# Kernel tuning notes

Measured on AMD Instinct MI355X. Metric: run time of the kernel, lower is better.

## Reference

```python
import jax, jax.numpy as jnp
import numpy as np

B, S, D = 4, 2048, 512
H = 8
DK = D // H  # 64, dim_q = dim_k
DFF = 2048
EPS = 1e-5


def _layernorm(x, g, b):
    mu = jnp.mean(x, axis=-1, keepdims=True)
    var = jnp.var(x, axis=-1, keepdims=True)
    return (x - mu) * jax.lax.rsqrt(var + EPS) * g + b


def setup_inputs() -> dict:
    key = jax.random.key(0)
    ks = jax.random.split(key, 12)
    s = 0.02
    return {
        "src": jax.random.normal(ks[0], (B, S, D), jnp.float32),
        "mask": jnp.ones((B, S, S), jnp.int32),
        # per-head projections (stacked over heads, faithful to separate Linear layers)
        "q_w": jax.random.normal(ks[1], (H, D, DK), jnp.float32) * s,
        "q_b": jnp.zeros((H, DK), jnp.float32),
        "k_w": jax.random.normal(ks[2], (H, D, DK), jnp.float32) * s,
        "k_b": jnp.zeros((H, DK), jnp.float32),
        "v_w": jax.random.normal(ks[3], (H, D, DK), jnp.float32) * s,
        "v_b": jnp.zeros((H, DK), jnp.float32),
        "o_w": jax.random.normal(ks[4], (H * DK, D), jnp.float32) * s,
        "o_b": jnp.zeros((D,), jnp.float32),
        "ln1_g": jnp.ones((D,), jnp.float32),
        "ln1_b": jnp.zeros((D,), jnp.float32),
        "w1": jax.random.normal(ks[5], (D, DFF), jnp.float32) * s,
        "b1": jnp.zeros((DFF,), jnp.float32),
        "w2": jax.random.normal(ks[6], (DFF, D), jnp.float32) * s,
        "b2": jnp.zeros((D,), jnp.float32),
        "ln2_g": jnp.ones((D,), jnp.float32),
        "ln2_b": jnp.zeros((D,), jnp.float32),
    }


def reference(src, mask, q_w, q_b, k_w, k_b, v_w, v_b, o_w, o_b,
              ln1_g, ln1_b, w1, b1, w2, b2, ln2_g, ln2_b):
    # --- multi-head self-attention (all heads vectorized) ---
    q = jnp.einsum('bsd,hde->bhse', src, q_w) + q_b[None, :, None, :]
    k = jnp.einsum('bsd,hde->bhse', src, k_w) + k_b[None, :, None, :]
    v = jnp.einsum('bsd,hde->bhse', src, v_w) + v_b[None, :, None, :]
    scores = jnp.einsum('bhqe,bhke->bhqk', q, k)  # [B,H,S,S]
    scores = jnp.where(mask[:, None, :, :] == 0, jnp.float32(-1e20), scores)
    scale = jnp.float32(DK) ** 0.5
    attn = jax.nn.softmax(scores / scale, axis=-1)
    ctx = jnp.einsum('bhqk,bhke->bhqe', attn, v)  # [B,H,S,DK]
    ctx = ctx.transpose(0, 2, 1, 3).reshape(B, S, H * DK)  # concat heads
    attn_out = ctx @ o_w + o_b
    x = _layernorm(src + attn_out, ln1_g, ln1_b)
    # --- feed forward ---
    ff = jax.nn.relu(x @ w1 + b1) @ w2 + b2
    return _layernorm(x + ff, ln2_g, ln2_b)
```

## Files before the change

### kernel.cpp

```cpp
#include <hip/hip_runtime.h>


typedef __bf16 bf16x8 __attribute__((ext_vector_type(8)));
typedef float f32x4 __attribute__((ext_vector_type(4)));
typedef unsigned short us4 __attribute__((ext_vector_type(4)));
typedef unsigned u32x4 __attribute__((ext_vector_type(4)));

__device__ __forceinline__ unsigned short f2bf(float f){
  unsigned u = __builtin_bit_cast(unsigned, f);
  u += 0x7fffu + ((u >> 16) & 1u);
  return (unsigned short)(u >> 16);
}
__device__ __forceinline__ float bf2f(unsigned short s){
  return __builtin_bit_cast(float, (unsigned)s << 16);
}

__device__ __forceinline__ unsigned cvt_pk_bf16(float lo, float hi){
  unsigned r;
  asm("v_cvt_pk_bf16_f32 %0, %1, %2" : "=v"(r) : "v"(lo), "v"(hi));
  return r;
}
__device__ __forceinline__ void plswap32(unsigned &a, unsigned &b){
  asm volatile("v_permlane32_swap_b32 %0, %1" : "+v"(a), "+v"(b));
}
__device__ __forceinline__ void plswap16(unsigned &a, unsigned &b){
  asm volatile("v_permlane16_swap_b32 %0, %1" : "+v"(a), "+v"(b));
}
__device__ __forceinline__ float exp2_hw(float x){
  float r;
  asm("v_exp_f32 %0, %1" : "=v"(r) : "v"(x));
  return r;
}

typedef const __attribute__((address_space(1))) void* gas_t;
typedef __attribute__((address_space(3))) void* las_t;
__device__ __forceinline__ void gl_lds16(const void* g, void* l){
  __builtin_amdgcn_global_load_lds((gas_t)g, (las_t)l, 16, 0, 0);
}

struct PrepSh { float t[32][33]; unsigned red[4]; };

__device__ __forceinline__ void wtrans_body(const float* __restrict__ in,
    unsigned short* __restrict__ out, int K, int N, int k0, int n0, int tid,
    float (*t)[33]){
  int tx = tid & 31, ty = tid >> 5;
  #pragma unroll
  for (int r = 0; r < 4; ++r)
    t[ty + 8*r][tx] = in[(size_t)(k0 + ty + 8*r)*N + n0 + tx];
  __syncthreads();
  #pragma unroll
  for (int r = 0; r < 4; ++r)
    out[(size_t)(n0 + ty + 8*r)*K + k0 + tx] = f2bf(t[tx][ty + 8*r]);
}

__global__ __launch_bounds__(256) void k_prep(
    const int* __restrict__ mask, const float* __restrict__ src,
    const float* __restrict__ qw, const float* __restrict__ kw, const float* __restrict__ vw,
    const float* __restrict__ qb, const float* __restrict__ kb, const float* __restrict__ vb,
    const float* __restrict__ ow, const float* __restrict__ w1, const float* __restrict__ w2,
    unsigned short* __restrict__ mb16, unsigned short* __restrict__ x_bf,
    unsigned short* __restrict__ wtqkv, float* __restrict__ bqkv,
    unsigned short* __restrict__ wto, unsigned short* __restrict__ wt1,
    unsigned short* __restrict__ wt2)
{
  __shared__ PrepSh sh;
  const int tid = threadIdx.x;
  int id = blockIdx.x;
  if (id < 256){
    const int bq = id & 127, half = id >> 7;
    const int b = bq >> 5, qt = bq & 31;
    const int* base = mask + (size_t)b*2048*2048 + (size_t)(qt*64 + (tid>>4)*4)*2048 + (tid&15)*4;
    unsigned bits = 0;
    for (int i = 0; i < 16; ++i){
      const int* p = base + (half*16 + i)*64;
      int ok = 1;
      #pragma unroll
      for (int r = 0; r < 4; ++r){
        int4 v = *reinterpret_cast<const int4*>(p + (size_t)r*2048);
        ok &= (v.x!=0)&(v.y!=0)&(v.z!=0)&(v.w!=0);
      }
      bits |= (unsigned)ok << i;
    }
    #pragma unroll
    for (int o = 1; o < 64; o <<= 1) bits &= __shfl_xor(bits, o);
    if ((tid & 63) == 0) sh.red[tid >> 6] = bits;
    __syncthreads();
    if (tid == 0) mb16[bq*2 + half] = (unsigned short)(sh.red[0]&sh.red[1]&sh.red[2]&sh.red[3]);
    return;
  }
  id -= 256;
  if (id < 4096){
    int i = id * 256 + tid;
    float4 v = reinterpret_cast<const float4*>(src)[i];
    us4 o = { f2bf(v.x), f2bf(v.y), f2bf(v.z), f2bf(v.w) };
    reinterpret_cast<us4*>(x_bf)[i] = o;
    return;
  }
  id -= 4096;
  if (id < 768){
    int z = id / 32, rem = id % 32, x = rem & 15, y = rem >> 4;
    int sel = z >> 3, h = z & 7;
    const float* in = (sel==0 ? qw : (sel==1 ? kw : vw)) + (size_t)h*512*64;
    unsigned short* o = wtqkv + ((size_t)(sel*512 + h*64)) * 512;
    wtrans_body(in, o, 512, 64, x*32, y*32, tid, sh.t);
    return;
  }
  id -= 768;
  if (id < 6){
    int n = id*256 + tid;
    if (n < 1536){ int sel = n >> 9, r = n & 511;
      bqkv[n] = (sel==0 ? qb : (sel==1 ? kb : vb))[r]; }
    return;
  }
  id -= 6;
  if (id < 256){
    wtrans_body(ow, wto, 512, 512, (id & 15)*32, (id >> 4)*32, tid, sh.t);
    return;
  }
  id -= 256;
  if (id < 1024){
    wtrans_body(w1, wt1, 512, 2048, (id & 15)*32, (id >> 4)*32, tid, sh.t);
    return;
  }
  id -= 1024;
  wtrans_body(w2, wt2, 2048, 512, (id & 63)*32, (id >> 6)*32, tid, sh.t);
}

template<int MODE>
__global__ __launch_bounds__(256, 3) void k_gemm(
    const unsigned short* __restrict__ A, const unsigned short* __restrict__ Bt,
    const float* __restrict__ bias, const float* __restrict__ resid,
    unsigned short* __restrict__ ob0, const unsigned short* __restrict__ ob1,
    unsigned short* __restrict__ ob2,
    float* __restrict__ of, int M, int N, int K)
{
  __shared__ unsigned short As[128*64];
  __shared__ unsigned short Bs[128*64];
  const int tid = threadIdx.x, lane = tid & 63, wid = tid >> 6;
  const int g = lane >> 4, lr = lane & 15;
  const int rowBase = blockIdx.x * 128, colBase = blockIdx.y * 128;
  const int wr = (wid >> 1) * 64, wc = (wid & 1) * 64;
  const int srow8 = lane >> 3;
  const int schunk = (lane & 7) ^ (srow8 & 7);
  const unsigned short* pA = A + (size_t)(rowBase + wid*32 + srow8)*K + schunk*8;
  const unsigned short* pB = Bt + (size_t)(colBase + wid*32 + srow8)*K + schunk*8;
  f32x4 acc[4][4] = {};
  for (int k0 = 0; k0 < K; k0 += 64){
    __syncthreads();
    #pragma unroll
    for (int t = 0; t < 4; ++t){
      gl_lds16(pA + (size_t)(t*8)*K + k0, &As[(wid*32 + t*8)*64]);
      gl_lds16(pB + (size_t)(t*8)*K + k0, &Bs[(wid*32 + t*8)*64]);
    }
    __syncthreads();
    #pragma unroll
    for (int ks = 0; ks < 2; ++ks){
      const int rc = ((ks*4 + g) ^ (lr & 7)) * 8;
      bf16x8 af[4], bfr[4];
      #pragma unroll
      for (int mi = 0; mi < 4; ++mi) af[mi]  = *reinterpret_cast<const bf16x8*>(&As[(wr + mi*16 + lr)*64 + rc]);
      #pragma unroll
      for (int ni = 0; ni < 4; ++ni) bfr[ni] = *reinterpret_cast<const bf16x8*>(&Bs[(wc + ni*16 + lr)*64 + rc]);
      __builtin_amdgcn_s_setprio(1);
      #pragma unroll
      for (int mi = 0; mi < 4; ++mi)
        #pragma unroll
        for (int ni = 0; ni < 4; ++ni)
          acc[mi][ni] = __builtin_amdgcn_mfma_f32_16x16x32_bf16(af[mi], bfr[ni], acc[mi][ni], 0, 0, 0);
      __builtin_amdgcn_s_setprio(0);
    }
  }
  float bv[4];
  #pragma unroll
  for (int ni = 0; ni < 4; ++ni) bv[ni] = bias[colBase + wc + ni*16 + lr];
  #pragma unroll
  for (int mi = 0; mi < 4; ++mi){
    #pragma unroll
    for (int ni = 0; ni < 4; ++ni){
      #pragma unroll
      for (int j = 0; j < 4; ++j){
        int m = rowBase + wr + mi*16 + g*4 + j;
        int n = colBase + wc + ni*16 + lr;
        float v = acc[mi][ni][j] + bv[ni];
        if constexpr (MODE == 0){
          int b = m >> 11, s = m & 2047;
          int sel = n >> 9, rr = n & 511, h = rr >> 6, e = rr & 63;
          size_t bh = (size_t)(b*8 + h);
          if (sel == 0)      ob0[(bh*2048 + s)*64 + e] = f2bf(v);
          else if (sel == 1) ((unsigned short*)ob1)[(bh*2048 + s)*64 + e] = f2bf(v);
          else               ob2[(bh*64 + e)*2048 + s] = f2bf(v);
        } else if constexpr (MODE == 1){
          of[(size_t)m*N + n] = v + resid[(size_t)m*N + n];
        } else if constexpr (MODE == 3){
          of[(size_t)m*N + n] = v + bf2f(ob1[(size_t)m*N + n]);
        } else {
          ob0[(size_t)m*N + n] = f2bf(v > 0.f ? v : 0.f);
        }
      }
    }
  }
}

__global__ __launch_bounds__(512) void k_attn(
    const unsigned short* __restrict__ Qb, const unsigned short* __restrict__ Kb,
    const unsigned short* __restrict__ Vt, const int* __restrict__ mask,
    const unsigned* __restrict__ mbits_p, unsigned short* __restrict__ ctx)
{
  __shared__ unsigned short Ks[2][8192];
  __shared__ unsigned short Vs[2][8192];
  const int tid = threadIdx.x, lane = tid & 63, wid = tid >> 6;
  const int g = lane >> 4, lr = lane & 15;
  const int qt = blockIdx.y, bh = blockIdx.x;
  const int b = bh >> 3, h = bh & 7;
  const int qw = qt * 128 + wid * 16;
  const unsigned mbits = mbits_p[b*32 + qt*2] & mbits_p[b*32 + qt*2 + 1];
  const size_t mbase = (size_t)b * 2048 * 2048;
  const float SC = 0.18033688f;

  const int l8 = lane >> 3, l7 = lane & 7, l16 = lane >> 4, l15 = lane & 15;
  const unsigned short* kg0 = Kb + (size_t)bh*2048*64 + ((size_t)(wid*16) + l8)*64 + ((l7 ^ (l8 & 7)))*8;
  const int vrow0 = wid*8 + l16, vrow1 = wid*8 + 4 + l16;
  const unsigned short* vg0 = Vt + (size_t)bh*64*2048 + (size_t)vrow0*2048 + ((l15 ^ (vrow0 & 15)))*8;
  const unsigned short* vg1 = Vt + (size_t)bh*64*2048 + (size_t)vrow1*2048 + ((l15 ^ (vrow1 & 15)))*8;

  #define STAGE(buf, t) do { \
    gl_lds16(kg0 + (size_t)(t)*8192,       &Ks[buf][(wid*16)*64]);    \
    gl_lds16(kg0 + (size_t)(t)*8192 + 512, &Ks[buf][(wid*16+8)*64]);  \
    gl_lds16(vg0 + (size_t)(t)*128,        &Vs[buf][(wid*8)*128]);    \
    gl_lds16(vg1 + (size_t)(t)*128,        &Vs[buf][(wid*8+4)*128]);  \
  } while(0)

  STAGE(0, 0);

  bf16x8 b_q[2];
  {
    const unsigned short* qp = Qb + ((size_t)bh*2048 + qw + lr)*64;
    b_q[0] = *reinterpret_cast<const bf16x8*>(qp + g*8);
    b_q[1] = *reinterpret_cast<const bf16x8*>(qp + 32 + g*8);
  }
  f32x4 acc[4] = {};
  float m_run = -3.0e38f, lp = 0.f;
  int cur = 0;
  __syncthreads();

  for (int kt = 0; kt < 16; ++kt){
    if (kt < 15) STAGE(cur^1, kt+1);
    const unsigned short* Kc = Ks[cur];
    const unsigned short* Vc = Vs[cur];
    f32x4 st[8];
    #pragma unroll
    for (int mk = 0; mk < 8; ++mk) st[mk] = f32x4{0.f,0.f,0.f,0.f};
    __builtin_amdgcn_s_setprio(1);
    #pragma unroll
    for (int mk = 0; mk < 8; ++mk)
      #pragma unroll
      for (int ks = 0; ks < 2; ++ks){
        bf16x8 kf = *reinterpret_cast<const bf16x8*>(
            &Kc[(mk*16 + lr)*64 + (((ks*4 + g) ^ (lr & 7)))*8]);
        st[mk] = __builtin_amdgcn_mfma_f32_16x16x32_bf16(kf, b_q[ks], st[mk], 0,0,0);
      }
    __builtin_amdgcn_s_setprio(0);
    if (((mbits >> (kt*2)) & 3u) != 3u){
      const int kk0 = kt * 128;
      #pragma unroll
      for (int mk = 0; mk < 8; ++mk)
        #pragma unroll
        for (int j = 0; j < 4; ++j){
          int kg = kk0 + mk*16 + g*4 + j;
          if (mask[mbase + (size_t)(qw + lr)*2048 + kg] == 0) st[mk][j] = -3.0e30f;
        }
    }
    float pm[8];
    #pragma unroll
    for (int mk = 0; mk < 8; ++mk)
      pm[mk] = fmaxf(fmaxf(st[mk][0], st[mk][1]), fmaxf(st[mk][2], st[mk][3]));
    float tA = fmaxf(fmaxf(pm[0], pm[1]), fmaxf(pm[2], pm[3]));
    float tB = fmaxf(fmaxf(pm[4], pm[5]), fmaxf(pm[6], pm[7]));
    float tm = fmaxf(tA, tB);
    tm = fmaxf(tm, __shfl_xor(tm, 16));
    tm = fmaxf(tm, __shfl_xor(tm, 32));
    float tms = tm * SC;
    if (!__all(tms <= m_run + 8.f)){
      float mnew = fmaxf(m_run, tms);
      float alpha = exp2_hw(m_run - mnew);
      lp *= alpha;
      #pragma unroll
      for (int ne = 0; ne < 4; ++ne)
        #pragma unroll
        for (int j = 0; j < 4; ++j) acc[ne][j] *= alpha;
      m_run = mnew;
    }
    unsigned wrd[8][2];
    float psA = 0.f, psB = 0.f;
    #pragma unroll
    for (int mk = 0; mk < 8; ++mk){
      float p0 = exp2_hw(__builtin_fmaf(st[mk][0], SC, -m_run));
      float p1 = exp2_hw(__builtin_fmaf(st[mk][1], SC, -m_run));
      float p2 = exp2_hw(__builtin_fmaf(st[mk][2], SC, -m_run));
      float p3 = exp2_hw(__builtin_fmaf(st[mk][3], SC, -m_run));
      psA += p0 + p2; psB += p1 + p3;
      wrd[mk][0] = cvt_pk_bf16(p0, p1);
      wrd[mk][1] = cvt_pk_bf16(p2, p3);
    }
    lp += psA + psB;
    bf16x8 pw[4];
    #pragma unroll
    for (int ks = 0; ks < 4; ++ks){
      unsigned a0w = wrd[2*ks][0], b0w = wrd[2*ks+1][0];
      unsigned a1w = wrd[2*ks][1], b1w = wrd[2*ks+1][1];
      plswap32(a0w, b0w); plswap16(a0w, b0w);
      plswap32(a1w, b1w); plswap16(a1w, b1w);
      u32x4 pk = { a0w, a1w, b0w, b1w };
      pw[ks] = __builtin_bit_cast(bf16x8, pk);
    }
    __builtin_amdgcn_s_setprio(1);
    #pragma unroll
    for (int ks = 0; ks < 4; ++ks)
      #pragma unroll
      for (int ne = 0; ne < 4; ++ne){
        bf16x8 vf = *reinterpret_cast<const bf16x8*>(
            &Vc[(ne*16 + lr)*128 + (((ks*4 + g) ^ lr))*8]);
        acc[ne] = __builtin_amdgcn_mfma_f32_16x16x32_bf16(vf, pw[ks], acc[ne], 0,0,0);
      }
    __builtin_amdgcn_s_setprio(0);
    if (kt < 15){
      __syncthreads();
      cur ^= 1;
    }
  }
  #undef STAGE
  float l = lp;
  l += __shfl_xor(l, 16);
  l += __shfl_xor(l, 32);
  float inv = 1.f / l;
  int q = qw + lr;
  #pragma unroll
  for (int ne = 0; ne < 4; ++ne){
    uint2 ow;
    ow.x = cvt_pk_bf16(acc[ne][0]*inv, acc[ne][1]*inv);
    ow.y = cvt_pk_bf16(acc[ne][2]*inv, acc[ne][3]*inv);
    *reinterpret_cast<uint2*>(&ctx[((size_t)b*2048 + q)*512 + h*64 + ne*16 + g*4]) = ow;
  }
}

__global__ __launch_bounds__(256) void k_ln(
    const float* __restrict__ in, const float* __restrict__ gma, const float* __restrict__ bta,
    float* __restrict__ of, unsigned short* __restrict__ ob)
{
  const int lane = threadIdx.x & 63, wid = threadIdx.x >> 6;
  const size_t row = (size_t)blockIdx.x * 4 + wid;
  const float* x = in + row * 512;
  const int e0 = lane * 8;
  float xv[8];
  *reinterpret_cast<float4*>(&xv[0]) = *reinterpret_cast<const float4*>(x + e0);
  *reinterpret_cast<float4*>(&xv[4]) = *reinterpret_cast<const float4*>(x + e0 + 4);
  float s = 0.f, ss = 0.f;
  #pragma unroll
  for (int i = 0; i < 8; ++i){ s += xv[i]; ss += xv[i]*xv[i]; }
  #pragma unroll
  for (int o = 1; o < 64; o <<= 1){ s += __shfl_xor(s, o); ss += __shfl_xor(ss, o); }
  float mu = s * (1.f/512.f);
  float var = ss * (1.f/512.f) - mu*mu;
  float rs = rsqrtf(var + 1e-5f);
  float gv[8], bv[8], y[8];
  *reinterpret_cast<float4*>(&gv[0]) = *reinterpret_cast<const float4*>(gma + e0);
  *reinterpret_cast<float4*>(&gv[4]) = *reinterpret_cast<const float4*>(gma + e0 + 4);
  *reinterpret_cast<float4*>(&bv[0]) = *reinterpret_cast<const float4*>(bta + e0);
  *reinterpret_cast<float4*>(&bv[4]) = *reinterpret_cast<const float4*>(bta + e0 + 4);
  #pragma unroll
  for (int i = 0; i < 8; ++i) y[i] = (xv[i]-mu)*rs*gv[i] + bv[i];
  if (of){
    *reinterpret_cast<float4*>(of + row*512 + e0)     = *reinterpret_cast<float4*>(&y[0]);
    *reinterpret_cast<float4*>(of + row*512 + e0 + 4) = *reinterpret_cast<float4*>(&y[4]);
  }
  if (ob){
    us4 o0 = { f2bf(y[0]), f2bf(y[1]), f2bf(y[2]), f2bf(y[3]) };
    us4 o1 = { f2bf(y[4]), f2bf(y[5]), f2bf(y[6]), f2bf(y[7]) };
    *reinterpret_cast<us4*>(ob + row*512 + e0)     = o0;
    *reinterpret_cast<us4*>(ob + row*512 + e0 + 4) = o1;
  }
}

extern "C" void kernel_launch(void* const* d_in, const int* in_sizes, int n_in,
                              void* d_out, int out_size, void* d_ws, size_t ws_size,
                              hipStream_t stream)
{
  const float* src  = (const float*)d_in[0];
  const int*   mask = (const int*)d_in[1];
  const float* q_w  = (const float*)d_in[2];
  const float* q_b  = (const float*)d_in[3];
  const float* k_w  = (const float*)d_in[4];
  const float* k_b  = (const float*)d_in[5];
  const float* v_w  = (const float*)d_in[6];
  const float* v_b  = (const float*)d_in[7];
  const float* o_w  = (const float*)d_in[8];
  const float* o_b  = (const float*)d_in[9];
  const float* ln1g = (const float*)d_in[10];
  const float* ln1b = (const float*)d_in[11];
  const float* w1   = (const float*)d_in[12];
  const float* b1   = (const float*)d_in[13];
  const float* w2   = (const float*)d_in[14];
  const float* b2   = (const float*)d_in[15];
  const float* ln2g = (const float*)d_in[16];
  const float* ln2b = (const float*)d_in[17];

  char* ws = (char*)d_ws;
  if (ws_size < 81795072) return;
  unsigned short* x_bf  = (unsigned short*)(ws + 0);
  unsigned short* wtqkv = (unsigned short*)(ws + 8388608);
  float*          bqkv  = (float*)(ws + 9961472);
  unsigned short* wto   = (unsigned short*)(ws + 9967616);
  unsigned short* wt1   = (unsigned short*)(ws + 10491904);
  unsigned short* wt2   = (unsigned short*)(ws + 12589056);
  unsigned short* Qb    = (unsigned short*)(ws + 14686208);
  unsigned short* Kb    = (unsigned short*)(ws + 23074816);
  unsigned short* Vt    = (unsigned short*)(ws + 31463424);
  unsigned short* ctx   = (unsigned short*)(ws + 39852032);
  unsigned short* ffb   = (unsigned short*)(ws + 14686208);
  float* res = (float*)(ws + 48240640);
  unsigned short* mb16 = (unsigned short*)(ws + 48240640);
  const unsigned* mb32 = (const unsigned*)(ws + 48240640);
  float* outf = (float*)d_out;

  k_prep<<<7430, 256, 0, stream>>>(mask, src, q_w, k_w, v_w, q_b, k_b, v_b,
                                   o_w, w1, w2, mb16, x_bf, wtqkv, bqkv, wto, wt1, wt2);

  k_gemm<0><<<dim3(64,12), 256, 0, stream>>>(x_bf, wtqkv, bqkv, nullptr,
                                             Qb, Kb, Vt, nullptr, 8192, 1536, 512);
  k_attn<<<dim3(32,16), 512, 0, stream>>>(Qb, Kb, Vt, mask, mb32, ctx);
  k_gemm<1><<<dim3(64,4), 256, 0, stream>>>(ctx, wto, o_b, src,
                                            nullptr, nullptr, nullptr, res, 8192, 512, 512);
  k_ln<<<2048, 256, 0, stream>>>(res, ln1g, ln1b, nullptr, x_bf);
  k_gemm<2><<<dim3(64,16), 256, 0, stream>>>(x_bf, wt1, b1, nullptr,
                                             ffb, nullptr, nullptr, nullptr, 8192, 2048, 512);
  k_gemm<3><<<dim3(64,4), 256, 0, stream>>>(ffb, wt2, b2, nullptr,
                                            nullptr, x_bf, nullptr, res, 8192, 512, 2048);
  k_ln<<<2048, 256, 0, stream>>>(res, ln2g, ln2b, outf, nullptr);
}
```

Before: 174.3 us.

## Split K across two warp groups in narrow-N GEMMs with LDS reduction

Adds a SPLIT template mode where a 512-thread block runs two 4-wave groups, each handling half of the K dimension with its own LDS tiles. The two partial accumulators are then summed through shared memory before the epilogue. It is applied to the output projection and FFN down-projection GEMMs, whose 256-block grids underfill the GPU. The aim is more waves per CU for latency hiding in these small grids, at the cost of doubled LDS, an extra reduction phase with barriers, and lower occupancy per block.

```diff
diff --git a/kernel.cpp b/kernel.cpp
--- a/kernel.cpp
+++ b/kernel.cpp
@@ -126,31 +126,34 @@
   wtrans_body(w2, wt2, 2048, 512, (id & 63)*32, (id >> 6)*32, tid, sh.t);
 }
 
-template<int MODE>
-__global__ __launch_bounds__(256, 3) void k_gemm(
+template<int MODE, int SPLIT>
+__global__ __launch_bounds__(SPLIT ? 512 : 256, SPLIT ? 2 : 3) void k_gemm(
     const unsigned short* __restrict__ A, const unsigned short* __restrict__ Bt,
     const float* __restrict__ bias, const float* __restrict__ resid,
     unsigned short* __restrict__ ob0, const unsigned short* __restrict__ ob1,
     unsigned short* __restrict__ ob2,
     float* __restrict__ of, int M, int N, int K)
 {
-  __shared__ unsigned short As[128*64];
-  __shared__ unsigned short Bs[128*64];
+  constexpr int NG = SPLIT ? 2 : 1;
+  __shared__ unsigned short As[NG][128*64];
+  __shared__ unsigned short Bs[NG][128*64];
   const int tid = threadIdx.x, lane = tid & 63, wid = tid >> 6;
+  const int w4 = wid & 3, kh = SPLIT ? (wid >> 2) : 0;
   const int g = lane >> 4, lr = lane & 15;
   const int rowBase = blockIdx.x * 128, colBase = blockIdx.y * 128;
-  const int wr = (wid >> 1) * 64, wc = (wid & 1) * 64;
+  const int wr = (w4 >> 1) * 64, wc = (w4 & 1) * 64;
   const int srow8 = lane >> 3;
   const int schunk = (lane & 7) ^ (srow8 & 7);
-  const unsigned short* pA = A + (size_t)(rowBase + wid*32 + srow8)*K + schunk*8;
-  const unsigned short* pB = Bt + (size_t)(colBase + wid*32 + srow8)*K + schunk*8;
+  const int Keff = SPLIT ? (K >> 1) : K;
+  const unsigned short* pA = A + (size_t)(rowBase + w4*32 + srow8)*K + kh*Keff + schunk*8;
+  const unsigned short* pB = Bt + (size_t)(colBase + w4*32 + srow8)*K + kh*Keff + schunk*8;
   f32x4 acc[4][4] = {};
-  for (int k0 = 0; k0 < K; k0 += 64){
+  for (int k0 = 0; k0 < Keff; k0 += 64){
     __syncthreads();
     #pragma unroll
     for (int t = 0; t < 4; ++t){
-      gl_lds16(pA + (size_t)(t*8)*K + k0, &As[(wid*32 + t*8)*64]);
-      gl_lds16(pB + (size_t)(t*8)*K + k0, &Bs[(wid*32 + t*8)*64]);
+      gl_lds16(pA + (size_t)(t*8)*K + k0, &As[kh][(w4*32 + t*8)*64]);
+      gl_lds16(pB + (size_t)(t*8)*K + k0, &Bs[kh][(w4*32 + t*8)*64]);
     }
     __syncthreads();
     #pragma unroll
@@ -158,9 +161,9 @@
       const int rc = ((ks*4 + g) ^ (lr & 7)) * 8;
       bf16x8 af[4], bfr[4];
       #pragma unroll
-      for (int mi = 0; mi < 4; ++mi) af[mi]  = *reinterpret_cast<const bf16x8*>(&As[(wr + mi*16 + lr)*64 + rc]);
-      #pragma unroll
-      for (int ni = 0; ni < 4; ++ni) bfr[ni] = *reinterpret_cast<const bf16x8*>(&Bs[(wc + ni*16 + lr)*64 + rc]);
+      for (int mi = 0; mi < 4; ++mi) af[mi]  = *reinterpret_cast<const bf16x8*>(&As[kh][(wr + mi*16 + lr)*64 + rc]);
+      #pragma unroll
+      for (int ni = 0; ni < 4; ++ni) bfr[ni] = *reinterpret_cast<const bf16x8*>(&Bs[kh][(wc + ni*16 + lr)*64 + rc]);
       __builtin_amdgcn_s_setprio(1);
       #pragma unroll
       for (int mi = 0; mi < 4; ++mi)
@@ -169,6 +172,35 @@
           acc[mi][ni] = __builtin_amdgcn_mfma_f32_16x16x32_bf16(af[mi], bfr[ni], acc[mi][ni], 0, 0, 0);
       __builtin_amdgcn_s_setprio(0);
     }
+  }
+  if constexpr (SPLIT){
+    float* xb = (float*)&As[0][0];
+    #pragma unroll
+    for (int p = 0; p < 2; ++p){
+      __syncthreads();
+      if (kh == 1 && (w4 >> 1) == p){
+        const int slot = w4 & 1;
+        #pragma unroll
+        for (int mi = 0; mi < 4; ++mi)
+          #pragma unroll
+          for (int ni = 0; ni < 4; ++ni)
+            #pragma unroll
+            for (int j = 0; j < 4; ++j)
+              xb[slot*4096 + (mi*16 + ni*4 + j)*64 + lane] = acc[mi][ni][j];
+      }
+      __syncthreads();
+      if (kh == 0 && (w4 >> 1) == p){
+        const int slot = w4 & 1;
+        #pragma unroll
+        for (int mi = 0; mi < 4; ++mi)
+          #pragma unroll
+          for (int ni = 0; ni < 4; ++ni)
+            #pragma unroll
+            for (int j = 0; j < 4; ++j)
+              acc[mi][ni][j] += xb[slot*4096 + (mi*16 + ni*4 + j)*64 + lane];
+      }
+    }
+    if (kh == 1) return;
   }
   float bv[4];
   #pragma unroll
@@ -425,15 +457,15 @@
   k_prep<<<7430, 256, 0, stream>>>(mask, src, q_w, k_w, v_w, q_b, k_b, v_b,
                                    o_w, w1, w2, mb16, x_bf, wtqkv, bqkv, wto, wt1, wt2);
 
-  k_gemm<0><<<dim3(64,12), 256, 0, stream>>>(x_bf, wtqkv, bqkv, nullptr,
-                                             Qb, Kb, Vt, nullptr, 8192, 1536, 512);
+  k_gemm<0,0><<<dim3(64,12), 256, 0, stream>>>(x_bf, wtqkv, bqkv, nullptr,
+                                               Qb, Kb, Vt, nullptr, 8192, 1536, 512);
   k_attn<<<dim3(32,16), 512, 0, stream>>>(Qb, Kb, Vt, mask, mb32, ctx);
-  k_gemm<1><<<dim3(64,4), 256, 0, stream>>>(ctx, wto, o_b, src,
-                                            nullptr, nullptr, nullptr, res, 8192, 512, 512);
+  k_gemm<1,1><<<dim3(64,4), 512, 0, stream>>>(ctx, wto, o_b, src,
+                                              nullptr, nullptr, nullptr, res, 8192, 512, 512);
   k_ln<<<2048, 256, 0, stream>>>(res, ln1g, ln1b, nullptr, x_bf);
-  k_gemm<2><<<dim3(64,16), 256, 0, stream>>>(x_bf, wt1, b1, nullptr,
-                                             ffb, nullptr, nullptr, nullptr, 8192, 2048, 512);
-  k_gemm<3><<<dim3(64,4), 256, 0, stream>>>(ffb, wt2, b2, nullptr,
-                                            nullptr, x_bf, nullptr, res, 8192, 512, 2048);
+  k_gemm<2,0><<<dim3(64,16), 256, 0, stream>>>(x_bf, wt1, b1, nullptr,
+                                               ffb, nullptr, nullptr, nullptr, 8192, 2048, 512);
+  k_gemm<3,1><<<dim3(64,4), 512, 0, stream>>>(ffb, wt2, b2, nullptr,
+                                              nullptr, x_bf, nullptr, res, 8192, 512, 2048);
   k_ln<<<2048, 256, 0, stream>>>(res, ln2g, ln2b, outf, nullptr);
 }
```

Result: faster. 168.1 us (-3.6%).
